# Kernel optimization log

Hardware: AMD Instinct MI355X
Metric: run time of the kernel (lower is better)

Reference implementation:

```python
import jax, jax.numpy as jnp
import numpy as np

B, C, L = 4, 512, 2048
H, D = 8, C // 8  # n_heads, attention_size


def conv1d_same(x, w, b):
    # x: [B, C, L], w: [Cout, Cin, 3], b: [Cout]; padding='same'
    y = jax.lax.conv_general_dilated(x, w, window_strides=(1,), padding='SAME',
                                     dimension_numbers=('NCH', 'OIH', 'NCH'))
    return y + b[None, :, None]


def setup_inputs() -> dict:
    key = jax.random.key(0)
    ks = jax.random.split(key, 11)
    s = 0.02
    inp = {
        'q': jax.random.normal(ks[0], (B, C, L), jnp.float32),
        'k': jax.random.normal(ks[1], (B, C, L), jnp.float32),
        'v': jax.random.normal(ks[2], (B, C, L), jnp.float32),
        'wq_w': jax.random.normal(ks[3], (C, C, 3), jnp.float32) * s,
        'wq_b': jnp.zeros((C,), jnp.float32),
        'wk_w': jax.random.normal(ks[4], (C, C, 3), jnp.float32) * s,
        'wk_b': jnp.zeros((C,), jnp.float32),
        'wv_w': jax.random.normal(ks[5], (C, C, 3), jnp.float32) * s,
        'wv_b': jnp.zeros((C,), jnp.float32),
        'fc_w': jax.random.normal(ks[6], (C, C, 3), jnp.float32) * s,
        'fc_b': jnp.zeros((C,), jnp.float32),
    }
    return inp


def reference(q, k, v, wq_w, wq_b, wk_w, wk_b, wv_w, wv_b, fc_w, fc_b):
    b = q.shape[0]
    # Faithful to torch: conv output [B,C,L] is row-major reshaped to [B,L,H,D]
    qh = conv1d_same(q, wq_w, wq_b).reshape(b, -1, H, D).transpose(0, 2, 1, 3)  # [B,H,L,D]
    kh = conv1d_same(k, wk_w, wk_b).reshape(b, -1, H, D).transpose(0, 2, 3, 1)  # [B,H,D,L]
    vh = conv1d_same(v, wv_w, wv_b).reshape(b, -1, H, D).transpose(0, 2, 1, 3)  # [B,H,L,D]
    # NOTE: original divides by attention_size D, not sqrt(D)
    attn = jax.nn.softmax(jnp.matmul(qh, kh) / D, axis=-1)  # [B,H,L,L]
    out = jnp.matmul(attn, vh)                               # [B,H,L,D]
    out = out.transpose(0, 2, 1, 3).reshape(b, H * D, -1)    # [B,C,L]
    return conv1d_same(out, fc_w, fc_b)
```

## Files before the change

### kernel.cpp

```cpp
#include <hip/hip_runtime.h>
#include <hip/hip_bf16.h>

#define BB 4
#define NH 8
#define HD 64
#define CC 512
#define LL 2048
#define KK 1536
#define LPAD 2050

#define QS 0.022542110013890054f

typedef float f32x4 __attribute__((ext_vector_type(4)));
typedef float f32x16 __attribute__((ext_vector_type(16)));
typedef short bf16x8 __attribute__((ext_vector_type(8)));

static __device__ __forceinline__ ushort f2bf(float f) {
  union { float f; unsigned u; } v; v.f = f;
  unsigned r = v.u + 0x7fffu + ((v.u >> 16) & 1u);
  return (ushort)(r >> 16);
}
static __device__ __forceinline__ void gload16(const ushort* g, ushort* l) {
  __builtin_amdgcn_global_load_lds((const __attribute__((address_space(1))) void*)g,
                                   (__attribute__((address_space(3))) void*)l, 16, 0, 0);
}

__global__ void prep_w(const float* __restrict__ w0, const float* __restrict__ w1,
                       const float* __restrict__ w2, const float* __restrict__ w3,
                       ushort* __restrict__ out)
{
  int i = blockIdx.x * 256 + threadIdx.x;
  const int per = CC * KK;
  if (i >= 4 * per) return;
  int cidx = i / per;
  int rem  = i - cidx * per;
  int co   = rem / KK;
  int kk   = rem - co * KK;
  int t = kk >> 9, ci = kk & 511;
  const float* w = (cidx == 0) ? w0 : (cidx == 1) ? w1 : (cidx == 2) ? w2 : w3;
  out[i] = f2bf(w[((size_t)co * CC + ci) * 3 + t]);
}

__device__ __forceinline__ void transpose_body(const float* __restrict__ xb,
                                               ushort* __restrict__ ob)
{
  const int c0 = blockIdx.y * 64;
  const int l0 = blockIdx.x * 64;
  const int tid = threadIdx.x;
  __shared__ ushort T[64 * 72];
  {
    const int rr = tid >> 4;
    const int f4 = tid & 15;
#pragma unroll
    for (int it = 0; it < 4; ++it) {
      const int cc = rr + it * 16;
      ushort s[4];
      float4 vv = *(const float4*)(xb + (size_t)(c0 + cc) * LL + l0 + f4 * 4);
      s[0] = f2bf(vv.x); s[1] = f2bf(vv.y); s[2] = f2bf(vv.z); s[3] = f2bf(vv.w);
      *(ushort4*)&T[cc * 72 + f4 * 4] = *(ushort4*)s;
    }
  }
  __syncthreads();
  {
    const int lr = tid >> 3;
    const int ch = tid & 7;
#pragma unroll
    for (int it = 0; it < 2; ++it) {
      const int ll = lr + it * 32;
      ushort tmp[8];
#pragma unroll
      for (int e = 0; e < 8; ++e) tmp[e] = T[(ch * 8 + e) * 72 + ll];
      *(uint4*)(ob + (size_t)(l0 + ll + 1) * CC + c0 + ch * 8) = *(uint4*)tmp;
    }
  }
  if (blockIdx.x == 0 && tid < 8) {
    uint4 z4 = make_uint4(0, 0, 0, 0);
    *(uint4*)(ob + c0 + tid * 8) = z4;
  }
  if (blockIdx.x == (LL / 64 - 1) && tid >= 248) {
    uint4 z4 = make_uint4(0, 0, 0, 0);
    *(uint4*)(ob + (size_t)(LPAD - 1) * CC + c0 + (tid - 248) * 8) = z4;
  }
}

__global__ __launch_bounds__(256, 4)
void transpose_k(const float* __restrict__ in, ushort* __restrict__ outT)
{
  const int b = blockIdx.z;
  transpose_body(in + (size_t)b * CC * LL, outT + (size_t)b * (LPAD * CC));
}

__global__ __launch_bounds__(256, 4)
void transpose3_k(const float* __restrict__ q, const float* __restrict__ k,
                  const float* __restrict__ v, ushort* __restrict__ xq,
                  ushort* __restrict__ xk, ushort* __restrict__ xv)
{
  const int z = blockIdx.z;
  const int b = z & 3, var = z >> 2;
  const float* in = (var == 0) ? q : (var == 1) ? k : v;
  ushort* out = (var == 0) ? xq : (var == 1) ? xk : xv;
  transpose_body(in + (size_t)b * CC * LL, out + (size_t)b * (LPAD * CC));
}

template<int BM>
__device__ __forceinline__ void conv_body(const ushort* __restrict__ xb,
                                          const ushort* __restrict__ Wt,
                                          const float* __restrict__ bias,
                                          void* __restrict__ outp, int mode, int b,
                                          float scale)
{
  const int co0 = blockIdx.y * BM;
  const int l0  = blockIdx.x * 128;
  const int tid = threadIdx.x;
  const int lane = tid & 63;
  const int w    = tid >> 6;
  const int col  = lane & 15, quad = lane >> 4;
  constexpr int MI = BM / 32;

  __shared__ ushort Asl[BM * 64];
  __shared__ ushort Bsl[128 * 64];

  const int sr = tid >> 3;
  const int g8 = ((tid & 7) ^ (sr & 7)) * 8;
  const ushort* ag  = Wt + (size_t)(co0 + sr) * KK + g8;
  const ushort* bg  = xb + (size_t)(l0 + sr) * CC + g8;
  ushort* alds = &Asl[tid * 8];
  ushort* blds = &Bsl[tid * 8];

  f32x4 acc[MI][4] = {};
  const int wm = (w & 1) * (BM / 2);
  const int wn = (w >> 1) * 64;
  const int c7 = col & 7;

  for (int k0 = 0; k0 < KK; k0 += 64) {
#pragma unroll
    for (int r2 = 0; r2 < MI; ++r2)
      gload16(ag + (size_t)(r2 * 32) * KK + k0, alds + r2 * 2048);
#pragma unroll
    for (int r2 = 0; r2 < 4; ++r2)
      gload16(bg + (size_t)(r2 * 32) * CC + k0, blds + r2 * 2048);
    __syncthreads();
#pragma unroll
    for (int kk = 0; kk < 2; ++kk) {
      bf16x8 af[MI], bfr[4];
#pragma unroll
      for (int i = 0; i < MI; ++i)
        af[i] = *(const bf16x8*)&Asl[(wm + i * 16 + col) * 64 + (((kk * 4 + quad) ^ c7) * 8)];
#pragma unroll
      for (int j = 0; j < 4; ++j)
        bfr[j] = *(const bf16x8*)&Bsl[(wn + j * 16 + col) * 64 + (((kk * 4 + quad) ^ c7) * 8)];
#pragma unroll
      for (int i = 0; i < MI; ++i)
#pragma unroll
        for (int j = 0; j < 4; ++j)
          acc[i][j] = __builtin_amdgcn_mfma_f32_16x16x32_bf16(af[i], bfr[j], acc[i][j], 0, 0, 0);
    }
    __syncthreads();
  }

#pragma unroll
  for (int i = 0; i < MI; ++i) {
#pragma unroll
    for (int r = 0; r < 4; ++r) {
      const int co = co0 + wm + i * 16 + quad * 4 + r;
      const float bi = bias[co];
#pragma unroll
      for (int j = 0; j < 4; ++j) {
        const int l = l0 + wn + j * 16 + col;
        const float y = (acc[i][j][r] + bi) * scale;
        if (mode == 0) {
          const int xx = (co << 2) + (l >> 9);
          const int hh = (l >> 6) & 7;
          const int dd = l & 63;
          ((ushort*)outp)[((size_t)(b * NH + hh) * LL + xx) * HD + dd] = f2bf(y);
        } else if (mode == 1) {
          const int xx = (co << 2) + (l >> 9);
          const int hh = (l >> 6) & 7;
          const int dd = l & 63;
          ((ushort*)outp)[((size_t)(b * NH + hh) * HD + dd) * LL + xx] = f2bf(y);
        } else {
          ((float*)outp)[(size_t)(b * CC + co) * LL + l] = y;
        }
      }
    }
  }
}

template<int BM>
__global__ __launch_bounds__(256, 3)
void conv_k(const ushort* __restrict__ xT, const ushort* __restrict__ Wt,
            const float* __restrict__ bias, void* __restrict__ outp, int mode,
            float scale)
{
  const int b = blockIdx.z;
  conv_body<BM>(xT + (size_t)b * (LPAD * CC), Wt, bias, outp, mode, b, scale);
}

__global__ __launch_bounds__(256, 3)
void conv3_k(const ushort* __restrict__ xq, const ushort* __restrict__ xk,
             const ushort* __restrict__ xv, const ushort* __restrict__ Wt,
             const float* __restrict__ b0, const float* __restrict__ b1,
             const float* __restrict__ b2, ushort* __restrict__ o0,
             ushort* __restrict__ o1, ushort* __restrict__ o2)
{
  const int z = blockIdx.z;
  const int b = z & 3, var = z >> 2;
  const ushort* xT = (var == 0) ? xq : (var == 1) ? xk : xv;
  const float* bias = (var == 0) ? b0 : (var == 1) ? b1 : b2;
  ushort* outp = (var == 0) ? o0 : (var == 1) ? o1 : o2;
  const float scale = (var == 0) ? QS : 1.0f;
  conv_body<128>(xT + (size_t)b * (LPAD * CC), Wt + (size_t)var * CC * KK, bias, outp,
                 (var == 2) ? 1 : 0, b, scale);
}

__global__ __launch_bounds__(256, 2)
void attn_k(const ushort* __restrict__ qh, const ushort* __restrict__ kh,
            const ushort* __restrict__ vt, ushort* __restrict__ obT)
{
  const int id   = blockIdx.x;
  const int xcd  = id & 7;
  const int slot = id >> 3;
  const int bh   = xcd * 4 + (slot >> 4);
  const int x0   = (slot & 15) * 128;
  const int b = bh >> 3, h = bh & 7;
  const int tid = threadIdx.x, lane = tid & 63, wv = tid >> 6;
  const int l31 = lane & 31, hi = lane >> 5, l7 = lane & 7;
  const int xloc = wv * 32 + l31;

  __shared__ ushort Kv[2][8192];
  __shared__ ushort Ps[128 * 72];

  const ushort* Qg = qh + (size_t)bh * (LL * HD);
  const ushort* Kg = kh + (size_t)bh * (LL * HD);
  const ushort* Vg = vt + (size_t)bh * (HD * LL);
  ushort* ob = obT + (size_t)b * (LPAD * CC);

  const int sr = tid >> 3;
  const int g8 = ((tid & 7) ^ (sr & 7)) * 8;

  bf16x8 qf[4];
#pragma unroll
  for (int ks = 0; ks < 4; ++ks)
    qf[ks] = *(const bf16x8*)(Qg + (size_t)(x0 + xloc) * HD + ks * 16 + hi * 8);

  const short one = (short)0x3F80;
  const bf16x8 ones = {one, one, one, one, one, one, one, one};

  f32x16 oacc[2] = {};
  f32x16 dacc = {};

  {
    ushort* kb = &Kv[0][tid * 8];
    gload16(Kg + (size_t)sr * HD + g8, kb);
    gload16(Kg + (size_t)(32 + sr) * HD + g8, kb + 2048);
    gload16(Vg + (size_t)sr * LL + g8, kb + 4096);
    gload16(Vg + (size_t)(32 + sr) * LL + g8, kb + 6144);
  }

  for (int yt = 0; yt < 32; ++yt) {
    const int cur = yt & 1;
    __syncthreads();
    if (yt + 1 < 32) {
      const int y1 = (yt + 1) * 64;
      ushort* kb = &Kv[1 - cur][tid * 8];
      gload16(Kg + (size_t)(y1 + sr) * HD + g8, kb);
      gload16(Kg + (size_t)(y1 + 32 + sr) * HD + g8, kb + 2048);
      gload16(Vg + (size_t)sr * LL + y1 + g8, kb + 4096);
      gload16(Vg + (size_t)(32 + sr) * LL + y1 + g8, kb + 6144);
    }
    const ushort* Kb = &Kv[cur][0];
    const ushort* Vb = &Kv[cur][4096];

    f32x16 sacc[2] = {};
#pragma unroll
    for (int mt = 0; mt < 2; ++mt) {
      const int row = mt * 32 + l31;
#pragma unroll
      for (int ks = 0; ks < 4; ++ks) {
        const int ch = (ks * 2 + hi) ^ l7;
        bf16x8 kf = *(const bf16x8*)&Kb[row * 64 + ch * 8];
        sacc[mt] = __builtin_amdgcn_mfma_f32_32x32x16_bf16(kf, qf[ks], sacc[mt], 0, 0, 0);
      }
    }

#pragma unroll
    for (int mt = 0; mt < 2; ++mt)
#pragma unroll
      for (int rq = 0; rq < 4; ++rq) {
        union { __hip_bfloat162 h2[2]; uint2 u; } pk;
        pk.h2[0] = __float22bfloat162_rn(make_float2(
            __builtin_amdgcn_exp2f(sacc[mt][rq * 4 + 0]),
            __builtin_amdgcn_exp2f(sacc[mt][rq * 4 + 1])));
        pk.h2[1] = __float22bfloat162_rn(make_float2(
            __builtin_amdgcn_exp2f(sacc[mt][rq * 4 + 2]),
            __builtin_amdgcn_exp2f(sacc[mt][rq * 4 + 3])));
        *(uint2*)&Ps[xloc * 72 + mt * 32 + rq * 8 + hi * 4] = pk.u;
      }

#pragma unroll
    for (int ks = 0; ks < 4; ++ks) {
      bf16x8 pa = *(const bf16x8*)&Ps[xloc * 72 + ks * 16 + hi * 8];
      dacc = __builtin_amdgcn_mfma_f32_32x32x16_bf16(pa, ones, dacc, 0, 0, 0);
#pragma unroll
      for (int nt = 0; nt < 2; ++nt) {
        const int rowd = nt * 32 + l31;
        const int ch = (ks * 2 + hi) ^ l7;
        bf16x8 vf = *(const bf16x8*)&Vb[rowd * 64 + ch * 8];
        oacc[nt] = __builtin_amdgcn_mfma_f32_32x32x16_bf16(pa, vf, oacc[nt], 0, 0, 0);
      }
    }
  }

#pragma unroll
  for (int reg = 0; reg < 16; ++reg) {
    const int xg = x0 + wv * 32 + (reg & 3) + 8 * (reg >> 2) + 4 * hi;
    const float inv = 1.f / dacc[reg];
#pragma unroll
    for (int nt = 0; nt < 2; ++nt) {
      const int d = nt * 32 + l31;
      const int flat = xg * 512 + h * 64 + d;
      const int c = flat >> 11, l = flat & 2047;
      ob[(size_t)(l + 1) * CC + c] = f2bf(oacc[nt][reg] * inv);
    }
  }
  if ((slot & 15) == 0 && tid < 128) {
    const int rw = tid >> 6;
    const int cc = h * 64 + (tid & 63);
    ob[(size_t)(rw ? (LPAD - 1) : 0) * CC + cc] = 0;
  }
}

extern "C" void kernel_launch(void* const* d_in, const int* in_sizes, int n_in,
                              void* d_out, int out_size, void* d_ws, size_t ws_size,
                              hipStream_t stream) {
  const float* q    = (const float*)d_in[0];
  const float* k    = (const float*)d_in[1];
  const float* v    = (const float*)d_in[2];
  const float* wq_w = (const float*)d_in[3];
  const float* wq_b = (const float*)d_in[4];
  const float* wk_w = (const float*)d_in[5];
  const float* wk_b = (const float*)d_in[6];
  const float* wv_w = (const float*)d_in[7];
  const float* wv_b = (const float*)d_in[8];
  const float* fc_w = (const float*)d_in[9];
  const float* fc_b = (const float*)d_in[10];

  char* ws = (char*)d_ws;
  const size_t WSZ = (size_t)CC * KK * sizeof(ushort);
  const size_t HSZ = (size_t)BB * NH * LL * HD * sizeof(ushort);
  const size_t XSZ = (size_t)BB * LPAD * CC * sizeof(ushort);
  const size_t FUSED_NEED = 4 * WSZ + 3 * HSZ + 3 * XSZ;

  ushort* Wt = (ushort*)(ws);
  prep_w<<<(4 * CC * KK + 255) / 256, 256, 0, stream>>>(wq_w, wk_w, wv_w, fc_w, Wt);

  if (ws_size >= FUSED_NEED) {
    ushort* qh  = (ushort*)(ws + 4 * WSZ);
    ushort* kh  = (ushort*)(ws + 4 * WSZ + HSZ);
    ushort* vt  = (ushort*)(ws + 4 * WSZ + 2 * HSZ);
    ushort* xTq = (ushort*)(ws + 4 * WSZ + 3 * HSZ);
    ushort* xTk = (ushort*)(ws + 4 * WSZ + 3 * HSZ + XSZ);
    ushort* xTv = (ushort*)(ws + 4 * WSZ + 3 * HSZ + 2 * XSZ);
    ushort* obT = xTq;

    transpose3_k<<<dim3(32, 8, 12), 256, 0, stream>>>(q, k, v, xTq, xTk, xTv);
    conv3_k<<<dim3(16, 4, 12), 256, 0, stream>>>(xTq, xTk, xTv, Wt,
                                                 wq_b, wk_b, wv_b, qh, kh, vt);
    attn_k<<<512, 256, 0, stream>>>(qh, kh, vt, obT);
    conv_k<64><<<dim3(16, 8, 4), 256, 0, stream>>>(obT, Wt + 3 * CC * KK, fc_b,
                                                   (float*)d_out, 2, 1.0f);
  } else {
    ushort* qh  = (ushort*)(ws + 4 * WSZ);
    ushort* kh  = (ushort*)(ws + 4 * WSZ + HSZ);
    ushort* vt  = (ushort*)(ws + 4 * WSZ + 2 * HSZ);
    ushort* xTb = (ushort*)(ws + 4 * WSZ + 3 * HSZ);
    ushort* obT = xTb;

    transpose_k<<<dim3(32, 8, 4), 256, 0, stream>>>(q, xTb);
    conv_k<128><<<dim3(16, 4, 4), 256, 0, stream>>>(xTb, Wt + 0 * CC * KK, wq_b, qh, 0, QS);
    transpose_k<<<dim3(32, 8, 4), 256, 0, stream>>>(k, xTb);
    conv_k<128><<<dim3(16, 4, 4), 256, 0, stream>>>(xTb, Wt + 1 * CC * KK, wk_b, kh, 0, 1.0f);
    transpose_k<<<dim3(32, 8, 4), 256, 0, stream>>>(v, xTb);
    conv_k<128><<<dim3(16, 4, 4), 256, 0, stream>>>(xTb, Wt + 2 * CC * KK, wv_b, vt, 1, 1.0f);
    attn_k<<<512, 256, 0, stream>>>(qh, kh, vt, obT);
    conv_k<64><<<dim3(16, 8, 4), 256, 0, stream>>>(obT, Wt + 3 * CC * KK, fc_b,
                                                   (float*)d_out, 2, 1.0f);
  }
}
```

Before: 252.2 us.

## Keep softmax P in registers via lane shuffles and sum denominator in scalars

The attention kernel no longer writes exp-scores to a shared-memory P tile and reads them back as the MFMA A operand. Instead it packs them to bf16 in registers and rearranges them across the two half-waves with __shfl_xor to match the A-operand layout. The softmax denominator is now accumulated as a plain fp32 per-lane sum plus one cross-half shuffle, replacing the extra MFMA against a ones vector. This cuts LDS traffic and the denominator MFMA from the inner loop, at the cost of extra shuffle/select instructions and a denominator summed from unrounded fp32 values instead of bf16 ones.

```diff
diff --git a/kernel.cpp b/kernel.cpp
--- a/kernel.cpp
+++ b/kernel.cpp
@@ -225,10 +225,9 @@
   const int b = bh >> 3, h = bh & 7;
   const int tid = threadIdx.x, lane = tid & 63, wv = tid >> 6;
   const int l31 = lane & 31, hi = lane >> 5, l7 = lane & 7;
-  const int xloc = wv * 32 + l31;
 
   __shared__ ushort Kv[2][8192];
-  __shared__ ushort Ps[128 * 72];
+  __shared__ float dbuf[4][32];
 
   const ushort* Qg = qh + (size_t)bh * (LL * HD);
   const ushort* Kg = kh + (size_t)bh * (LL * HD);
@@ -241,13 +240,10 @@
   bf16x8 qf[4];
 #pragma unroll
   for (int ks = 0; ks < 4; ++ks)
-    qf[ks] = *(const bf16x8*)(Qg + (size_t)(x0 + xloc) * HD + ks * 16 + hi * 8);
-
-  const short one = (short)0x3F80;
-  const bf16x8 ones = {one, one, one, one, one, one, one, one};
+    qf[ks] = *(const bf16x8*)(Qg + (size_t)(x0 + wv * 32 + l31) * HD + ks * 16 + hi * 8);
 
   f32x16 oacc[2] = {};
-  f32x16 dacc = {};
+  float dsum = 0.f;
 
   {
     ushort* kb = &Kv[0][tid * 8];
@@ -283,38 +279,57 @@
       }
     }
 
+    uint pw[2][4][2];
 #pragma unroll
     for (int mt = 0; mt < 2; ++mt)
 #pragma unroll
       for (int rq = 0; rq < 4; ++rq) {
-        union { __hip_bfloat162 h2[2]; uint2 u; } pk;
-        pk.h2[0] = __float22bfloat162_rn(make_float2(
-            __builtin_amdgcn_exp2f(sacc[mt][rq * 4 + 0]),
-            __builtin_amdgcn_exp2f(sacc[mt][rq * 4 + 1])));
-        pk.h2[1] = __float22bfloat162_rn(make_float2(
-            __builtin_amdgcn_exp2f(sacc[mt][rq * 4 + 2]),
-            __builtin_amdgcn_exp2f(sacc[mt][rq * 4 + 3])));
-        *(uint2*)&Ps[xloc * 72 + mt * 32 + rq * 8 + hi * 4] = pk.u;
+        const float e0 = __builtin_amdgcn_exp2f(sacc[mt][rq * 4 + 0]);
+        const float e1 = __builtin_amdgcn_exp2f(sacc[mt][rq * 4 + 1]);
+        const float e2 = __builtin_amdgcn_exp2f(sacc[mt][rq * 4 + 2]);
+        const float e3 = __builtin_amdgcn_exp2f(sacc[mt][rq * 4 + 3]);
+        dsum += (e0 + e1) + (e2 + e3);
+        union { __hip_bfloat162 h2; uint u; } a, c;
+        a.h2 = __float22bfloat162_rn(make_float2(e0, e1));
+        c.h2 = __float22bfloat162_rn(make_float2(e2, e3));
+        pw[mt][rq][0] = a.u;
+        pw[mt][rq][1] = c.u;
       }
 
 #pragma unroll
     for (int ks = 0; ks < 4; ++ks) {
-      bf16x8 pa = *(const bf16x8*)&Ps[xloc * 72 + ks * 16 + hi * 8];
-      dacc = __builtin_amdgcn_mfma_f32_32x32x16_bf16(pa, ones, dacc, 0, 0, 0);
+      const int mt = ks >> 1, rqA = (ks & 1) * 2;
+      union { bf16x8 v; uint u[4]; } pa;
+#pragma unroll
+      for (int w = 0; w < 2; ++w) {
+        const uint A  = pw[mt][rqA][w];
+        const uint Bv = pw[mt][rqA + 1][w];
+        const uint V  = hi ? A : Bv;
+        const uint X  = (uint)__shfl_xor((int)V, 32, 64);
+        pa.u[w]     = hi ? X : A;
+        pa.u[w + 2] = hi ? Bv : X;
+      }
 #pragma unroll
       for (int nt = 0; nt < 2; ++nt) {
         const int rowd = nt * 32 + l31;
         const int ch = (ks * 2 + hi) ^ l7;
         bf16x8 vf = *(const bf16x8*)&Vb[rowd * 64 + ch * 8];
-        oacc[nt] = __builtin_amdgcn_mfma_f32_32x32x16_bf16(pa, vf, oacc[nt], 0, 0, 0);
+        oacc[nt] = __builtin_amdgcn_mfma_f32_32x32x16_bf16(pa.v, vf, oacc[nt], 0, 0, 0);
       }
     }
   }
+
+  const float dtot = dsum + __shfl_xor(dsum, 32, 64);
+  if (hi == 0) dbuf[wv][l31] = dtot;
+  f32x4 rd[4];
+#pragma unroll
+  for (int q = 0; q < 4; ++q)
+    rd[q] = *(const f32x4*)&dbuf[wv][q * 8 + 4 * hi];
 
 #pragma unroll
   for (int reg = 0; reg < 16; ++reg) {
     const int xg = x0 + wv * 32 + (reg & 3) + 8 * (reg >> 2) + 4 * hi;
-    const float inv = 1.f / dacc[reg];
+    const float inv = 1.f / rd[reg >> 2][reg & 3];
 #pragma unroll
     for (int nt = 0; nt < 2; ++nt) {
       const int d = nt * 32 + l31;
```

After: 260.7 us. +3.4%, slower.
